# Kernel optimization log

Hardware: AMD Instinct MI355X
Metric: run time of the kernel (lower is better)

## Reference

```python
import jax, jax.numpy as jnp
import numpy as np

B, S, HID, NH, HD, SKV = 2, 2048, 1024, 16, 64, 2048

def setup_inputs() -> dict:
    key = jax.random.key(0)
    ks = jax.random.split(key, 9)
    s = 0.02
    return {
        "hidden_states": jax.random.normal(ks[0], (B, S, HID), jnp.float32),
        "kvs": jax.random.normal(ks[1], (2, B, NH, SKV, HD), jnp.float32),
        "Wq": jax.random.normal(ks[2], (HID, HID), jnp.float32) * s,
        "bq": jax.random.normal(ks[3], (HID,), jnp.float32) * s,
        "Wk": jax.random.normal(ks[4], (HID, HID), jnp.float32) * s,
        "bk": jax.random.normal(ks[5], (HID,), jnp.float32) * s,
        "Wv": jax.random.normal(ks[6], (HID, HID), jnp.float32) * s,
        "bv": jax.random.normal(ks[7], (HID,), jnp.float32) * s,
        "kv_weight": jnp.ones((), jnp.float32),
    }

def _heads(x):
    # [B,S,HID] -> [B,NH,S,HD]
    return x.reshape(B, -1, NH, HD).transpose(0, 2, 1, 3)

def reference(hidden_states, kvs, Wq, bq, Wk, bk, Wv, bv, kv_weight):
    scale = HD ** (-0.5)
    # torch nn.Linear: y = x @ W.T + b
    q = _heads((hidden_states @ Wq.T + bq) * scale)        # [B,NH,S,HD]
    k = _heads(hidden_states @ Wk.T + bk)
    v = _heads(hidden_states @ Wv.T + bv)
    k = jnp.concatenate([kv_weight * kvs[0], k], axis=2)   # [B,NH,SKV+S,HD]
    v = jnp.concatenate([kv_weight * kvs[1], v], axis=2)
    # module scales twice: q * d^-0.5 then scores / sqrt(d)
    scores = jnp.einsum("bhqd,bhkd->bhqk", q, k) * scale
    probs = jax.nn.softmax(scores, axis=-1)
    # dropout(p=0.1) is identity in eval mode
    ctx = jnp.einsum("bhqk,bhkd->bhqd", probs, v)          # [B,NH,S,HD]
    ctx = ctx.transpose(0, 2, 1, 3).reshape(B, S, HID)
    return ctx
```

## Files before the change

### kernel.cpp

```cpp
#include <hip/hip_runtime.h>
#include <hip/hip_bf16.h>


typedef __bf16 bf16x8 __attribute__((ext_vector_type(8)));
typedef float f32x4 __attribute__((ext_vector_type(4)));
typedef float f32x16 __attribute__((ext_vector_type(16)));
typedef unsigned int uint4v __attribute__((ext_vector_type(4)));
typedef unsigned short u16x4 __attribute__((ext_vector_type(4)));

#define QSCALE 0.0225421100138900525f

static __device__ __forceinline__ unsigned short bf16b(float f) {
  return __builtin_bit_cast(unsigned short, __float2bfloat16(f));
}
static __device__ __forceinline__ unsigned pk2(float lo, float hi) {
  return (unsigned)bf16b(lo) | ((unsigned)bf16b(hi) << 16);
}
static __device__ __forceinline__ bf16x8 ld16s(const unsigned short* p) {
  return __builtin_bit_cast(bf16x8, *(const uint4v*)p);
}
static __device__ __forceinline__ float fexp2(float x) {
  float r; asm("v_exp_f32 %0, %1" : "=v"(r) : "v"(x)); return r;
}

typedef __attribute__((address_space(1))) const void gas_void;
typedef __attribute__((address_space(3))) void las_void;
static __device__ __forceinline__ void gload_lds16(const void* g, void* l) {
  __builtin_amdgcn_global_load_lds((gas_void*)g, (las_void*)l, 16, 0, 0);
}

__global__ __launch_bounds__(256) void prep_convert(
    const float* __restrict__ hs, const float* __restrict__ wq,
    const float* __restrict__ wk, const float* __restrict__ wv,
    const float* __restrict__ kv0, const float* __restrict__ kvw,
    unsigned short* __restrict__ hsb, unsigned short* __restrict__ wb,
    unsigned short* __restrict__ kbuf) {
  long i = ((long)blockIdx.x * 256 + threadIdx.x) * 4;
  const float* src; unsigned short* dst; float s = 1.0f;
  if (i < 4194304)      { src = hs + i;           dst = hsb + i; }
  else if (i < 5242880) { src = wq + (i-4194304); dst = wb + (i-4194304); }
  else if (i < 6291456) { src = wk + (i-5242880); dst = wb + 1048576 + (i-5242880); }
  else if (i < 7340032) { src = wv + (i-6291456); dst = wb + 2097152 + (i-6291456); }
  else { long j = i - 7340032; s = *kvw;
         long bh = j >> 17, r = j & 131071;
         src = kv0 + j; dst = kbuf + (bh << 18) + r; }
  float4 v = *(const float4*)src;
  u16x4 o = { bf16b(v.x*s), bf16b(v.y*s), bf16b(v.z*s), bf16b(v.w*s) };
  *(u16x4*)dst = o;
}

__global__ __launch_bounds__(256) void qkv_gemm(
    const unsigned short* __restrict__ A, const unsigned short* __restrict__ W,
    const float* __restrict__ bq, const float* __restrict__ bk, const float* __restrict__ bv,
    unsigned short* __restrict__ qb, unsigned short* __restrict__ kbuf,
    unsigned short* __restrict__ vtb) {
  int mode = blockIdx.y;
  const unsigned short* Wm = W + mode * 1048576;
  const float* bias = (mode == 0) ? bq : ((mode == 1) ? bk : bv);
  int mt = blockIdx.x >> 3, nt = blockIdx.x & 7;
  int m0 = mt << 7, n0 = nt << 7;
  int wid = threadIdx.x >> 6, ln = threadIdx.x & 63;
  int wr = wid >> 1, wc = wid & 1;
  __shared__ unsigned short As[2][4096], Bs[2][4096];

  f32x4 acc[4][4] = {};

  auto stage = [&](int bb, int kt) {
    #pragma unroll
    for (int i = 0; i < 2; ++i) {
      int c = i*256 + wid*64 + ln;
      int row = c >> 2, sl = c & 3;
      int lb = (i*256 + wid*64) * 8;
      gload_lds16(A  + (long)(m0 + row)*1024 + kt*32 + sl*8, &As[bb][lb]);
      gload_lds16(Wm + (long)(n0 + row)*1024 + kt*32 + sl*8, &Bs[bb][lb]);
    }
  };

  stage(0, 0);
  __syncthreads();
  int buf = 0;
  for (int kt = 0; kt < 32; ++kt) {
    if (kt < 31) stage(buf ^ 1, kt + 1);
    bf16x8 a[4], b[4];
    int rsel = (ln & 15), ksel = (ln >> 4) * 8;
    #pragma unroll
    for (int x = 0; x < 4; ++x) {
      a[x] = ld16s(&As[buf][(wr*64 + x*16 + rsel)*32 + ksel]);
      b[x] = ld16s(&Bs[buf][(wc*64 + x*16 + rsel)*32 + ksel]);
    }
    __builtin_amdgcn_s_setprio(1);
    #pragma unroll
    for (int x = 0; x < 4; ++x)
      #pragma unroll
      for (int y = 0; y < 4; ++y)
        acc[x][y] = __builtin_amdgcn_mfma_f32_16x16x32_bf16(a[x], b[y], acc[x][y], 0, 0, 0);
    __builtin_amdgcn_s_setprio(0);
    __syncthreads();
    buf ^= 1;
  }

  float bias4[4];
  #pragma unroll
  for (int y = 0; y < 4; ++y) bias4[y] = bias[n0 + wc*64 + y*16 + (ln & 15)];

  if (mode == 2) {
    #pragma unroll
    for (int x = 0; x < 4; ++x)
      #pragma unroll
      for (int y = 0; y < 4; ++y) {
        int gm = m0 + wr*64 + x*16 + (ln >> 4)*4;
        int gn = n0 + wc*64 + y*16 + (ln & 15);
        int bb = gm >> 11, s = gm & 2047, h = gn >> 6, d = gn & 63;
        long bh = bb*16 + h;
        u16x4 o = { bf16b(acc[x][y][0] + bias4[y]), bf16b(acc[x][y][1] + bias4[y]),
                    bf16b(acc[x][y][2] + bias4[y]), bf16b(acc[x][y][3] + bias4[y]) };
        *(u16x4*)(vtb + bh*262144 + (long)d*4096 + 2048 + s) = o;
      }
  } else {
    #pragma unroll
    for (int x = 0; x < 4; ++x)
      #pragma unroll
      for (int y = 0; y < 4; ++y)
        #pragma unroll
        for (int r = 0; r < 4; ++r) {
          int gm = m0 + wr*64 + x*16 + (ln >> 4)*4 + r;
          int gn = n0 + wc*64 + y*16 + (ln & 15);
          float v = acc[x][y][r] + bias4[y];
          int bb = gm >> 11, s = gm & 2047, h = gn >> 6, d = gn & 63;
          long bh = bb*16 + h;
          if (mode == 0) qb[(bh*2048 + s)*64 + d]          = bf16b(v * QSCALE);
          else           kbuf[(bh*4096 + 2048 + s)*64 + d] = bf16b(v);
        }
  }
}

__global__ __launch_bounds__(256) void transpose_v(
    const float* __restrict__ src, unsigned short* __restrict__ dst,
    const float* __restrict__ scale_ptr) {
  __shared__ float tile[64 * 65];
  int bh = blockIdx.x >> 5;
  int s0 = (blockIdx.x & 31) << 6;
  int tid = threadIdx.x;
  float sc = *scale_ptr;
  long sb = ((long)bh*2048 + s0) * 64;
  #pragma unroll
  for (int j = 0; j < 4; ++j) {
    int c = tid + j*256;
    int row = c >> 4, sl = c & 15;
    float4 v = *(const float4*)(src + sb + row*64 + sl*4);
    float* p = &tile[row*65 + sl*4];
    p[0] = v.x*sc; p[1] = v.y*sc; p[2] = v.z*sc; p[3] = v.w*sc;
  }
  __syncthreads();
  int d = tid >> 2, kc = tid & 3;
  unsigned short u16[16];
  #pragma unroll
  for (int t = 0; t < 16; ++t) u16[t] = bf16b(tile[(kc*16 + t)*65 + d]);
  uint4v o0v = { (unsigned)u16[0] | ((unsigned)u16[1]<<16), (unsigned)u16[2] | ((unsigned)u16[3]<<16),
                 (unsigned)u16[4] | ((unsigned)u16[5]<<16), (unsigned)u16[6] | ((unsigned)u16[7]<<16) };
  uint4v o1v = { (unsigned)u16[8] | ((unsigned)u16[9]<<16), (unsigned)u16[10] | ((unsigned)u16[11]<<16),
                 (unsigned)u16[12] | ((unsigned)u16[13]<<16), (unsigned)u16[14] | ((unsigned)u16[15]<<16) };
  long db = (long)bh*262144 + (long)d*4096 + s0 + kc*16;
  *(uint4v*)(dst + db) = o0v;
  *(uint4v*)(dst + db + 8) = o1v;
}

template <int NT, bool DIRECT>
__global__ __launch_bounds__(256) void attn(
    const unsigned short* __restrict__ qb, const unsigned short* __restrict__ kb,
    const unsigned short* __restrict__ vtb, float* __restrict__ out,
    float* __restrict__ po, float* __restrict__ pl) {
  int tilei = blockIdx.x, bh = blockIdx.y, sp = blockIdx.z;
  int keyoff = sp * NT * 64;
  int wid = threadIdx.x >> 6, ln = threadIdx.x & 63;
  int lo = ln & 31, hi = ln >> 5;
  __shared__ unsigned short Ks[2][4096], Vs[2][4096];

  const unsigned short* kg = kb  + (long)bh * 262144;
  const unsigned short* vg = vtb + (long)bh * 262144;
  int qbase = tilei*256 + wid*64;
  bf16x8 qf[2][4];
  #pragma unroll
  for (int g = 0; g < 2; ++g) {
    const unsigned short* qrow = qb + ((long)bh*2048 + qbase + g*32 + lo) * 64;
    #pragma unroll
    for (int ds = 0; ds < 4; ++ds) qf[g][ds] = ld16s(qrow + ds*16 + hi*8);
  }

  f32x16 o[2][2] = {};
  f32x4 lacc[2] = {};

  auto stage = [&](int bb, int t) {
    int key0 = keyoff + (t << 6);
    #pragma unroll
    for (int i = 0; i < 2; ++i) {
      int c = i*256 + wid*64 + ln;
      int row = c >> 3, sl = c & 7;
      int swz = (sl ^ (row & 7)) * 8;
      int lb = (i*256 + wid*64) * 8;
      gload_lds16(kg + (long)(key0 + row)*64 + swz, &Ks[bb][lb]);
      gload_lds16(vg + (long)row*4096 + key0 + swz, &Vs[bb][lb]);
    }
  };

  stage(0, 0);
  __syncthreads();
  int buf = 0;
  for (int t = 0; t < NT; ++t) {
    if (t < NT-1) stage(buf ^ 1, t + 1);
    const unsigned short* Kt = Ks[buf];
    const unsigned short* Vt = Vs[buf];
    #pragma unroll
    for (int cc = 0; cc < 2; ++cc) {
      int key = cc*32 + lo;
      bf16x8 kf[4];
      #pragma unroll
      for (int ds = 0; ds < 4; ++ds)
        kf[ds] = ld16s(&Kt[key*64 + ((2*ds + hi) ^ (key & 7))*8]);
      bf16x8 pf[2][2];
      #pragma unroll
      for (int g = 0; g < 2; ++g) {
        f32x16 st = {};
        __builtin_amdgcn_s_setprio(1);
        #pragma unroll
        for (int ds = 0; ds < 4; ++ds)
          st = __builtin_amdgcn_mfma_f32_32x32x16_bf16(kf[ds], qf[g][ds], st, 0, 0, 0);
        __builtin_amdgcn_s_setprio(0);
        float p[16];
        #pragma unroll
        for (int r = 0; r < 16; ++r) p[r] = fexp2(st[r]);
        f32x4 l4 = { (p[0]+p[1]) + (p[2]+p[3]),   (p[4]+p[5]) + (p[6]+p[7]),
                     (p[8]+p[9]) + (p[10]+p[11]), (p[12]+p[13]) + (p[14]+p[15]) };
        lacc[g] += l4;
        #pragma unroll
        for (int ks = 0; ks < 2; ++ks) {
          unsigned X  = pk2(p[8*ks+0], p[8*ks+1]);
          unsigned X2 = pk2(p[8*ks+2], p[8*ks+3]);
          unsigned Y  = pk2(p[8*ks+4], p[8*ks+5]);
          unsigned Y2 = pk2(p[8*ks+6], p[8*ks+7]);
          asm("v_permlane32_swap_b32 %0, %1" : "+v"(X), "+v"(Y));
          asm("v_permlane32_swap_b32 %0, %1" : "+v"(X2), "+v"(Y2));
          uint4v pw = { X, X2, Y, Y2 };
          pf[g][ks] = __builtin_bit_cast(bf16x8, pw);
        }
      }
      #pragma unroll
      for (int ks = 0; ks < 2; ++ks) {
        int slv = ((cc*4 + 2*ks + hi) ^ (lo & 7)) * 8;
        bf16x8 vf0 = ld16s(&Vt[lo*64 + slv]);
        bf16x8 vf1 = ld16s(&Vt[(32 + lo)*64 + slv]);
        __builtin_amdgcn_s_setprio(1);
        #pragma unroll
        for (int g = 0; g < 2; ++g) {
          o[g][0] = __builtin_amdgcn_mfma_f32_32x32x16_bf16(vf0, pf[g][ks], o[g][0], 0, 0, 0);
          o[g][1] = __builtin_amdgcn_mfma_f32_32x32x16_bf16(vf1, pf[g][ks], o[g][1], 0, 0, 0);
        }
        __builtin_amdgcn_s_setprio(0);
      }
    }
    __syncthreads();
    buf ^= 1;
  }

  #pragma unroll
  for (int g = 0; g < 2; ++g) {
    float lsum = (lacc[g][0] + lacc[g][1]) + (lacc[g][2] + lacc[g][3]);
    lsum += __shfl_xor(lsum, 32, 64);
    int q = qbase + g*32 + lo;
    if constexpr (DIRECT) {
      float inv = 1.0f / lsum;
      int bb = bh >> 4, h = bh & 15;
      float* orow = out + ((long)bb*2048 + q)*1024 + h*64;
      #pragma unroll
      for (int dh = 0; dh < 2; ++dh) {
        #pragma unroll
        for (int gg = 0; gg < 4; ++gg) {
          f32x4 vv = { o[g][dh][4*gg]*inv, o[g][dh][4*gg+1]*inv,
                       o[g][dh][4*gg+2]*inv, o[g][dh][4*gg+3]*inv };
          *(f32x4*)(orow + dh*32 + gg*8 + 4*hi) = vv;
        }
      }
    } else {
      float* prow = po + (((long)sp*32 + bh)*2048 + q) * 64;
      #pragma unroll
      for (int dh = 0; dh < 2; ++dh) {
        #pragma unroll
        for (int gg = 0; gg < 4; ++gg) {
          f32x4 vv = { o[g][dh][4*gg], o[g][dh][4*gg+1], o[g][dh][4*gg+2], o[g][dh][4*gg+3] };
          *(f32x4*)(prow + dh*32 + gg*8 + 4*hi) = vv;
        }
      }
      if (hi == 0) pl[((long)sp*32 + bh)*2048 + q] = lsum;
    }
  }
}

__global__ __launch_bounds__(256) void combine2(
    const float* __restrict__ po, const float* __restrict__ pl, float* __restrict__ out) {
  long flat = ((long)blockIdx.x * 256 + threadIdx.x) * 4;
  int bh = (int)(flat >> 17);
  int rem = (int)(flat & 131071);
  int q = rem >> 6, d = rem & 63;
  f32x4 a = *(const f32x4*)(po + flat);
  f32x4 b = *(const f32x4*)(po + 4194304 + flat);
  float l = pl[bh*2048 + q] + pl[65536 + bh*2048 + q];
  float inv = 1.0f / l;
  f32x4 r = { (a[0]+b[0])*inv, (a[1]+b[1])*inv, (a[2]+b[2])*inv, (a[3]+b[3])*inv };
  *(f32x4*)(out + ((long)(bh >> 4)*2048 + q)*1024 + (bh & 15)*64 + d) = r;
}

extern "C" void kernel_launch(void* const* d_in, const int* in_sizes, int n_in,
                              void* d_out, int out_size, void* d_ws, size_t ws_size,
                              hipStream_t stream) {
  const float* hs  = (const float*)d_in[0];
  const float* kvs = (const float*)d_in[1];
  const float* Wq  = (const float*)d_in[2];
  const float* bq  = (const float*)d_in[3];
  const float* Wk  = (const float*)d_in[4];
  const float* bk  = (const float*)d_in[5];
  const float* Wv  = (const float*)d_in[6];
  const float* bv  = (const float*)d_in[7];
  const float* kvw = (const float*)d_in[8];
  float* out = (float*)d_out;

  char* w = (char*)d_ws;
  unsigned short* hsb  = (unsigned short*)(w);
  unsigned short* wb   = (unsigned short*)(w + (8l  << 20));
  unsigned short* qbuf = (unsigned short*)(w + (14l << 20));
  unsigned short* kbuf = (unsigned short*)(w + (22l << 20));
  unsigned short* vtb  = (unsigned short*)(w + (38l << 20));
  float* po = (float*)(w + (64l << 20));
  float* pl = (float*)(w + (128l << 20));

  const float* kv0 = kvs;
  const float* kv1 = kvs + 4194304;

  prep_convert<<<dim3(11264), dim3(256), 0, stream>>>(hs, Wq, Wk, Wv, kv0, kvw, hsb, wb, kbuf);
  qkv_gemm<<<dim3(256, 3), dim3(256), 0, stream>>>(hsb, wb, bq, bk, bv, qbuf, kbuf, vtb);
  transpose_v<<<dim3(1024), dim3(256), 0, stream>>>(kv1, vtb, kvw);

  if (ws_size >= (129ul << 20)) {
    attn<32, false><<<dim3(8, 32, 2), dim3(256), 0, stream>>>(qbuf, kbuf, vtb, nullptr, po, pl);
    combine2<<<dim3(4096), dim3(256), 0, stream>>>(po, pl, out);
  } else {
    attn<64, true><<<dim3(8, 32, 1), dim3(256), 0, stream>>>(qbuf, kbuf, vtb, out, nullptr, nullptr);
  }
}
```

Measured before the change: 255.2 us.

## Load K and V fragments directly from global memory, dropping LDS staging

Removes the double-buffered LDS staging of K and V tiles along with the per-tile barriers. Each wave now reads its K and V MFMA fragments straight from global memory with 16-byte loads. This removes LDS traffic and synchronisation and frees shared memory, which may raise occupancy. In exchange, the four waves of a block each fetch the same K/V data through cache, and the loads are no longer prefetched a tile ahead, so global latency may be exposed to the MFMA loop.

```diff
diff --git a/kernel.cpp b/kernel.cpp
--- a/kernel.cpp
+++ b/kernel.cpp
@@ -174,7 +174,6 @@
   int keyoff = sp * NT * 64;
   int wid = threadIdx.x >> 6, ln = threadIdx.x & 63;
   int lo = ln & 31, hi = ln >> 5;
-  __shared__ unsigned short Ks[2][4096], Vs[2][4096];
 
   const unsigned short* kg = kb  + (long)bh * 262144;
   const unsigned short* vg = vtb + (long)bh * 262144;
@@ -190,33 +189,18 @@
   f32x16 o[2][2] = {};
   f32x4 lacc[2] = {};
 
-  auto stage = [&](int bb, int t) {
-    int key0 = keyoff + (t << 6);
-    #pragma unroll
-    for (int i = 0; i < 2; ++i) {
-      int c = i*256 + wid*64 + ln;
-      int row = c >> 3, sl = c & 7;
-      int swz = (sl ^ (row & 7)) * 8;
-      int lb = (i*256 + wid*64) * 8;
-      gload_lds16(kg + (long)(key0 + row)*64 + swz, &Ks[bb][lb]);
-      gload_lds16(vg + (long)row*4096 + key0 + swz, &Vs[bb][lb]);
-    }
-  };
-
-  stage(0, 0);
-  __syncthreads();
-  int buf = 0;
+  const unsigned short* krow = kg + (long)(keyoff + lo)*64 + hi*8;
+  const unsigned short* vrow0 = vg + (long)lo*4096 + keyoff + hi*8;
+  const unsigned short* vrow1 = vg + (long)(32+lo)*4096 + keyoff + hi*8;
+
   for (int t = 0; t < NT; ++t) {
-    if (t < NT-1) stage(buf ^ 1, t + 1);
-    const unsigned short* Kt = Ks[buf];
-    const unsigned short* Vt = Vs[buf];
     #pragma unroll
     for (int cc = 0; cc < 2; ++cc) {
-      int key = cc*32 + lo;
+      long kbase = (long)(t*64 + cc*32) * 64;
       bf16x8 kf[4];
       #pragma unroll
       for (int ds = 0; ds < 4; ++ds)
-        kf[ds] = ld16s(&Kt[key*64 + ((2*ds + hi) ^ (key & 7))*8]);
+        kf[ds] = ld16s(krow + kbase + ds*16);
       bf16x8 pf[2][2];
       #pragma unroll
       for (int g = 0; g < 2; ++g) {
@@ -246,9 +230,9 @@
       }
       #pragma unroll
       for (int ks = 0; ks < 2; ++ks) {
-        int slv = ((cc*4 + 2*ks + hi) ^ (lo & 7)) * 8;
-        bf16x8 vf0 = ld16s(&Vt[lo*64 + slv]);
-        bf16x8 vf1 = ld16s(&Vt[(32 + lo)*64 + slv]);
+        int vcol = t*64 + cc*32 + ks*16;
+        bf16x8 vf0 = ld16s(vrow0 + vcol);
+        bf16x8 vf1 = ld16s(vrow1 + vcol);
         __builtin_amdgcn_s_setprio(1);
         #pragma unroll
         for (int g = 0; g < 2; ++g) {
@@ -258,8 +242,6 @@
         __builtin_amdgcn_s_setprio(0);
       }
     }
-    __syncthreads();
-    buf ^= 1;
   }
 
   #pragma unroll
```

Measured after the change: 283.5 us. 11.1% more time.
